# Optimization experiments

Measured on AMD Instinct MI355X. Metric: run time of the kernel, lower is better.

## Reference

```python
import jax, jax.numpy as jnp
import numpy as np

B, S, D, N, H = 2, 1024, 1024, 16, 64
R = 2 * S          # max relative length
EPS = 1e-9
INF = 1000000.0
SHIFT = 1          # q_len == context_len branch


def _forward(query, key, value, r, cls_mask, Wq, Wk, bk, Wv, bv, Wo, bo,
             r_w_bias, r_r_bias, r_kernel, r_s_bias, seg_embed, ln_gamma, ln_beta,
             token_type_mat, attention_mask):
    scale = 1.0 / np.sqrt(H).astype(np.float32)
    q = (query @ Wq).reshape(B, S, N, H) * scale          # [b,s,n,h]
    k = (key @ Wk + bk).reshape(B, S, N, H)
    v = (value @ Wv + bv).reshape(B, S, N, H)

    # content score
    content = jnp.einsum('binh,bjnh->bnij', q + r_w_bias * scale, k)

    # relative positional score with shift-gather trick
    r_head = jnp.einsum('td,dnh->tnh', r, r_kernel)        # [2S,n,h]
    pos = jnp.einsum('binh,tnh->bnit', q + r_r_bias * scale, r_head)  # [b,n,s,2S]
    pos = pos.reshape(B, N, R, S)[:, :, SHIFT:, :].reshape(B, N, S, R - SHIFT)[..., :S]
    pos = pos * cls_mask

    # token-type (segment) score: seg_embed[0]=diff, seg_embed[1]=same
    tt_bias = jnp.einsum('binh,snh->bnis', q + r_s_bias * scale, seg_embed)  # [b,n,s,2]
    diff, same = tt_bias[..., :1], tt_bias[..., 1:]
    tt = jnp.where(token_type_mat[:, None], same, diff) * cls_mask           # [b,n,s,s]

    mask = attention_mask.astype(jnp.float32)[:, None, None]                 # [b,1,1,s]
    attn_score = content + pos + tt - INF * (1.0 - mask)
    attn_prob = jax.nn.softmax(attn_score, axis=-1)

    attn_vec = jnp.einsum('bnij,bjnh->binh', attn_prob, v).reshape(B, S, N * H)
    attn_out = attn_vec @ Wo + bo

    x = query + attn_out
    mu = jnp.mean(x, axis=-1, keepdims=True)
    var = jnp.mean(jnp.square(x - mu), axis=-1, keepdims=True)
    return (x - mu) * jax.lax.rsqrt(var + EPS) * ln_gamma + ln_beta


def setup_inputs() -> dict:
    rng = jax.random.key(0)
    ks = jax.random.split(rng, 16)
    init = 0.02
    inp = {
        'query': jax.random.normal(ks[0], (B, S, D), jnp.float32),
        'key':   jax.random.normal(ks[1], (B, S, D), jnp.float32),
        'value': jax.random.normal(ks[2], (B, S, D), jnp.float32),
        'r':     jax.random.normal(ks[3], (R, D), jnp.float32),
        'cls_mask': jnp.ones((S, S), jnp.float32),
        'Wq': jax.random.normal(ks[4], (D, N * H), jnp.float32) * init,
        'Wk': jax.random.normal(ks[5], (D, N * H), jnp.float32) * init,
        'bk': jnp.zeros((N * H,), jnp.float32),
        'Wv': jax.random.normal(ks[6], (D, N * H), jnp.float32) * init,
        'bv': jnp.zeros((N * H,), jnp.float32),
        'Wo': jax.random.normal(ks[7], (N * H, D), jnp.float32) * init,
        'bo': jnp.zeros((D,), jnp.float32),
        'r_w_bias': jax.random.normal(ks[8], (N, H), jnp.float32) * init,
        'r_r_bias': jax.random.normal(ks[9], (N, H), jnp.float32) * init,
        'r_kernel': jax.random.normal(ks[10], (D, N, H), jnp.float32) * init,
        'r_s_bias': jax.random.normal(ks[11], (N, H), jnp.float32) * init,
        'seg_embed': jax.random.normal(ks[12], (2, N, H), jnp.float32) * init,
        'ln_gamma': jnp.ones((D,), jnp.float32),
        'ln_beta': jnp.zeros((D,), jnp.float32),
        'token_type_mat': jax.random.randint(ks[13], (B, S, S), 0, 2).astype(bool),
        'attention_mask': jax.random.randint(ks[14], (B, S), 0, 2).astype(jnp.int32),
    }
    return inp


def reference(query, key, value, r, cls_mask, Wq, Wk, bk, Wv, bv, Wo, bo,
              r_w_bias, r_r_bias, r_kernel, r_s_bias, seg_embed, ln_gamma, ln_beta,
              token_type_mat, attention_mask):
    return _forward(query, key, value, r, cls_mask, Wq, Wk, bk, Wv, bv, Wo, bo,
                    r_w_bias, r_r_bias, r_kernel, r_s_bias, seg_embed, ln_gamma, ln_beta,
                    token_type_mat, attention_mask)
```

## Files before the change

### kernel.cpp

```cpp
#include <hip/hip_runtime.h>

#define S_ 1024

typedef short short8 __attribute__((ext_vector_type(8)));
typedef float floatx4 __attribute__((ext_vector_type(4)));

static __device__ __forceinline__ float b2f(ushort u) {
    union { float f; unsigned int i; } x; x.i = ((unsigned int)u) << 16; return x.f;
}
static __device__ __forceinline__ ushort f2b(float f) {
    union { float f; unsigned int i; } x; x.f = f;
    unsigned int r = (x.i + 0x7fffu + ((x.i >> 16) & 1u)) >> 16;
    return (ushort)r;
}
static __device__ __forceinline__ void async_copy16(ushort* lds, const ushort* g) {
    __builtin_amdgcn_global_load_lds((const __attribute__((address_space(1))) void*)g,
                                     (__attribute__((address_space(3))) void*)lds, 16, 0, 0);
}
template <int CTRL>
static __device__ __forceinline__ float dpp_radd(float x) {
    union { float f; int i; } a, b;
    a.f = x;
    b.i = __builtin_amdgcn_mov_dpp(a.i, CTRL, 0xf, 0xf, true);
    return x + b.f;
}

struct PreArgs {
    const float* csrc[4]; ushort* cdst[4];
    const float* tsrc[5]; ushort* tdst[5];
    const int* ttm; unsigned long long* ttb;
    const int* am;  unsigned long long* amb;
};
__global__ __launch_bounds__(256) void pre_kernel(PreArgs a) {
    int z = blockIdx.z, tid = threadIdx.x;
    if (z < 4) {
        const float* s = a.csrc[z];
        ushort* d = a.cdst[z];
        size_t idx = ((size_t)blockIdx.x * 256 + tid) * 8;
        float4 f0 = *(const float4*)&s[idx];
        float4 f1 = *(const float4*)&s[idx + 4];
        alignas(16) ushort u[8] = {f2b(f0.x), f2b(f0.y), f2b(f0.z), f2b(f0.w),
                                   f2b(f1.x), f2b(f1.y), f2b(f1.z), f2b(f1.w)};
        *(uint4*)&d[idx] = *(uint4*)u;
    } else if (z < 9) {
        const float* src = a.tsrc[z - 4];
        ushort* dst = a.tdst[z - 4];
        __shared__ float tile[32][33];
        int bx = (blockIdx.x & 31) * 32, by = (blockIdx.x >> 5) * 32;
        int tx = tid & 31, ty = tid >> 5;
#pragma unroll
        for (int i = 0; i < 32; i += 8)
            tile[ty + i][tx] = src[(size_t)(by + ty + i) * 1024 + bx + tx];
        __syncthreads();
#pragma unroll
        for (int i = 0; i < 32; i += 8)
            dst[(size_t)(bx + ty + i) * 1024 + by + tx] = f2b(tile[tx][ty + i]);
    } else {
        int w = tid >> 6, lane = tid & 63;
        int waveid = blockIdx.x * 4 + w;
#pragma unroll
        for (int t = 0; t < 8; t++) {
            int word = waveid * 8 + t;
            unsigned long long m = __ballot(a.ttm[(size_t)word * 64 + lane] != 0);
            if (lane == 0) a.ttb[word] = m;
        }
        if (blockIdx.x == 0 && w == 0) {
            for (int t = 0; t < 32; t++) {
                unsigned long long m = __ballot(a.am[(size_t)t * 64 + lane] != 0);
                if (lane == 0) a.amb[t] = m;
            }
        }
    }
}

struct ProjArgs {
    const ushort* A[4];
    const ushort* BT[4];
    const float* bias[4];
    ushort* C[4];
    float scale[4];
};
__global__ __launch_bounds__(256, 2) void gemm_proj(ProjArgs args) {
    int z = blockIdx.z;
    const ushort* A = args.A[z];
    const ushort* BT = args.BT[z];
    const float* bias = args.bias[z];
    ushort* C = args.C[z];
    float scale = args.scale[z];

    __shared__ alignas(16) ushort As[128 * 64];
    __shared__ alignas(16) ushort Bs[128 * 64];
    int n0 = blockIdx.x * 128, m0 = blockIdx.y * 128;
    int tid = threadIdx.x, lane = tid & 63, w = tid >> 6;
    int wm = (w >> 1) * 64, wn = (w & 1) * 64;
    int li = lane & 15, q4 = lane >> 4;
    int lrow = lane >> 3, lu = (lane & 7) ^ lrow;
    floatx4 acc[4][4] = {};
    for (int k0 = 0; k0 < 1024; k0 += 64) {
        __syncthreads();
#pragma unroll
        for (int t = 0; t < 4; t++) {
            int c = 4 * w + t;
            const ushort* ga = &A[(size_t)(m0 + 8 * c + lrow) * 1024 + k0 + 8 * lu];
            async_copy16(&As[c * 512 + lane * 8], ga);
            const ushort* gb = &BT[(size_t)(n0 + 8 * c + lrow) * 1024 + k0 + 8 * lu];
            async_copy16(&Bs[c * 512 + lane * 8], gb);
        }
        __syncthreads();
        short8 af[2][4], bf[2][4];
#pragma unroll
        for (int kk = 0; kk < 2; kk++) {
#pragma unroll
            for (int ms = 0; ms < 4; ms++)
                af[kk][ms] = *(const short8*)&As[(wm + 16 * ms + li) * 64 +
                                                (((4 * kk + q4) ^ (li & 7)) * 8)];
#pragma unroll
            for (int ns = 0; ns < 4; ns++)
                bf[kk][ns] = *(const short8*)&Bs[(wn + 16 * ns + li) * 64 +
                                                (((4 * kk + q4) ^ (li & 7)) * 8)];
        }
#pragma unroll
        for (int kk = 0; kk < 2; kk++)
#pragma unroll
            for (int ms = 0; ms < 4; ms++)
#pragma unroll
                for (int ns = 0; ns < 4; ns++)
                    acc[ms][ns] = __builtin_amdgcn_mfma_f32_16x16x32_bf16(af[kk][ms], bf[kk][ns],
                                                                          acc[ms][ns], 0, 0, 0);
    }
#pragma unroll
    for (int ns = 0; ns < 4; ns++) {
        int col = n0 + wn + 16 * ns + li;
        float bv = bias ? bias[col] : 0.f;
#pragma unroll
        for (int ms = 0; ms < 4; ms++)
#pragma unroll
            for (int rg = 0; rg < 4; rg++) {
                int row = m0 + wm + 16 * ms + 4 * q4 + rg;
                C[(size_t)row * 1024 + col] = f2b(acc[ms][ns][rg] * scale + bv);
            }
    }
}

__global__ __launch_bounds__(256, 2) void gemm_out(const ushort* __restrict__ A,
                                                   const ushort* __restrict__ BT,
                                                   const float* __restrict__ bias,
                                                   const float* __restrict__ resid,
                                                   float* __restrict__ X) {
    __shared__ alignas(16) ushort As[64 * 64];
    __shared__ alignas(16) ushort Bs[64 * 64];
    int n0 = blockIdx.x * 64, m0 = blockIdx.y * 64;
    int tid = threadIdx.x, lane = tid & 63, w = tid >> 6;
    int wm = (w >> 1) * 32, wn = (w & 1) * 32;
    int li = lane & 15, q4 = lane >> 4;
    int lrow = lane >> 3, lu = (lane & 7) ^ lrow;
    floatx4 acc[2][2] = {};
    for (int k0 = 0; k0 < 1024; k0 += 64) {
        __syncthreads();
#pragma unroll
        for (int t = 0; t < 2; t++) {
            int c = 2 * w + t;
            const ushort* ga = &A[(size_t)(m0 + 8 * c + lrow) * 1024 + k0 + 8 * lu];
            async_copy16(&As[c * 512 + lane * 8], ga);
            const ushort* gb = &BT[(size_t)(n0 + 8 * c + lrow) * 1024 + k0 + 8 * lu];
            async_copy16(&Bs[c * 512 + lane * 8], gb);
        }
        __syncthreads();
        short8 af[2][2], bf[2][2];
#pragma unroll
        for (int kk = 0; kk < 2; kk++) {
#pragma unroll
            for (int ms = 0; ms < 2; ms++)
                af[kk][ms] = *(const short8*)&As[(wm + 16 * ms + li) * 64 +
                                                (((4 * kk + q4) ^ (li & 7)) * 8)];
#pragma unroll
            for (int ns = 0; ns < 2; ns++)
                bf[kk][ns] = *(const short8*)&Bs[(wn + 16 * ns + li) * 64 +
                                                (((4 * kk + q4) ^ (li & 7)) * 8)];
        }
#pragma unroll
        for (int kk = 0; kk < 2; kk++)
#pragma unroll
            for (int ms = 0; ms < 2; ms++)
#pragma unroll
                for (int ns = 0; ns < 2; ns++)
                    acc[ms][ns] = __builtin_amdgcn_mfma_f32_16x16x32_bf16(af[kk][ms], bf[kk][ns],
                                                                          acc[ms][ns], 0, 0, 0);
    }
#pragma unroll
    for (int ns = 0; ns < 2; ns++) {
        int col = n0 + wn + 16 * ns + li;
        float bv = bias[col];
#pragma unroll
        for (int ms = 0; ms < 2; ms++)
#pragma unroll
            for (int rg = 0; rg < 4; rg++) {
                int row = m0 + wm + 16 * ms + 4 * q4 + rg;
                X[(size_t)row * 1024 + col] = acc[ms][ns][rg] + bv + resid[(size_t)row * 1024 + col];
            }
    }
}

__global__ __launch_bounds__(256, 2) void attn_kernel(
    const ushort* __restrict__ qg, const ushort* __restrict__ kg,
    const ushort* __restrict__ vg, const ushort* __restrict__ rh,
    const float* __restrict__ rwb, const float* __restrict__ rrb,
    const float* __restrict__ rsb, const float* __restrict__ seg,
    const unsigned long long* __restrict__ ttb, const unsigned long long* __restrict__ amb,
    ushort* __restrict__ av) {
    __shared__ alignas(16) ushort vt[64][72];
    __shared__ alignas(16) ushort pb[4][16][72];

    int lid = blockIdx.x + 16 * blockIdx.y + 256 * blockIdx.z;
    int g = lid & 7, tt_ = lid >> 3;
    int i0 = (tt_ & 15) * 64;
    int slice = 4 * g + (tt_ >> 4);
    int n = slice & 15, b = slice >> 4;

    int tid = threadIdx.x, lane = tid & 63, w = tid >> 6;
    int li = lane & 15, q4 = lane >> 4;
    const float SC = 0.125f;
    const int kRow = b * S_;

    short8 aw0, aw1, ar0, ar1;
    float ttd_l[4], tts_l[4];
    {
        int qrow = kRow + i0 + 16 * w + li;
        int h0 = n * 64 + 8 * q4;
        const ushort* qp = &qg[(size_t)qrow * 1024 + h0];
        alignas(16) ushort t0[8], t1[8];
        *(uint4*)t0 = *(const uint4*)qp;
        *(uint4*)t1 = *(const uint4*)(qp + 32);
        alignas(16) ushort w0[8], w1[8], r0[8], r1[8];
        float d = 0.f, s = 0.f;
#pragma unroll
        for (int e = 0; e < 8; e++) {
            float qv0 = b2f(t0[e]), qv1 = b2f(t1[e]);
            int ha = h0 + e, hb = h0 + 32 + e;
            w0[e] = f2b(qv0 + rwb[ha] * SC);
            w1[e] = f2b(qv1 + rwb[hb] * SC);
            r0[e] = f2b(qv0 + rrb[ha] * SC);
            r1[e] = f2b(qv1 + rrb[hb] * SC);
            float s0 = qv0 + rsb[ha] * SC, s1 = qv1 + rsb[hb] * SC;
            d += s0 * seg[ha] + s1 * seg[hb];
            s += s0 * seg[1024 + ha] + s1 * seg[1024 + hb];
        }
        aw0 = *(short8*)w0; aw1 = *(short8*)w1;
        ar0 = *(short8*)r0; ar1 = *(short8*)r1;
        d += __shfl_xor(d, 16, 64); d += __shfl_xor(d, 32, 64);
        s += __shfl_xor(s, 16, 64); s += __shfl_xor(s, 32, 64);
#pragma unroll
        for (int r = 0; r < 4; r++) {
            int srcl = (lane & 48) | (4 * q4 + r);
            ttd_l[r] = __shfl(d, srcl, 64);
            tts_l[r] = __shfl(s, srcl, 64);
        }
    }

    floatx4 o[4] = {};
    float l_i[4] = {0.f, 0.f, 0.f, 0.f};

    int g8 = tid >> 5, jp = tid & 31;

    short8 kf0[4], kf1[4], rf0[5], rf1[5];
    uint4 pv0, pv1;
    unsigned long long ptb[4], pamb;

#define LOAD_K(J0)                                                                     \
    {                                                                                  \
        _Pragma("unroll") for (int s_ = 0; s_ < 4; s_++) {                             \
            const ushort* kp =                                                         \
                &kg[(size_t)(kRow + (J0) + 16 * s_ + li) * 1024 + n * 64 + 8 * q4];    \
            kf0[s_] = *(const short8*)kp;                                              \
            kf1[s_] = *(const short8*)(kp + 32);                                       \
        }                                                                              \
    }
#define LOAD_R(J0)                                                                     \
    {                                                                                  \
        _Pragma("unroll") for (int s_ = 0; s_ < 5; s_++) {                             \
            int t_ = 1024 + (J0) - i0 - 15 - 16 * w + 16 * s_ + li;                    \
            if (t_ > 2047) t_ = 2047;                                                  \
            const ushort* rp = &rh[(size_t)t_ * 1024 + n * 64 + 8 * q4];               \
            rf0[s_] = *(const short8*)rp;                                              \
            rf1[s_] = *(const short8*)(rp + 32);                                       \
        }                                                                              \
    }
#define LOAD_VTB(J0)                                                                   \
    {                                                                                  \
        const ushort* vp = &vg[(size_t)(kRow + (J0) + 2 * jp) * 1024 + n * 64 + 8 * g8]; \
        pv0 = *(const uint4*)vp;                                                       \
        pv1 = *(const uint4*)(vp + 1024);                                              \
        int wj_ = (J0) >> 6;                                                           \
        pamb = amb[b * 16 + wj_];                                                      \
        _Pragma("unroll") for (int r_ = 0; r_ < 4; r_++)                               \
            ptb[r_] = ttb[((size_t)kRow + i0 + 16 * w + 4 * q4 + r_) * 16 + wj_];      \
    }
    LOAD_K(0);
    LOAD_R(0);
    LOAD_VTB(0);

    for (int j0 = 0; j0 < 1024; j0 += 64) {
        __syncthreads();
        {
            alignas(16) ushort au[8], bu[8];
            *(uint4*)au = pv0; *(uint4*)bu = pv1;
#pragma unroll
            for (int e = 0; e < 8; e++) {
                unsigned int val = (unsigned int)au[e] | ((unsigned int)bu[e] << 16);
                *(unsigned int*)&vt[8 * g8 + e][2 * jp] = val;
            }
        }
        unsigned long long ambw = pamb;
        unsigned long long tb[4] = {ptb[0], ptb[1], ptb[2], ptb[3]};
        __syncthreads();
        bool more = (j0 + 64 < 1024);
        if (more) LOAD_VTB(j0 + 64);

        floatx4 cs[4] = {};
#pragma unroll
        for (int s = 0; s < 4; s++) {
            cs[s] = __builtin_amdgcn_mfma_f32_16x16x32_bf16(aw0, kf0[s], cs[s], 0, 0, 0);
            cs[s] = __builtin_amdgcn_mfma_f32_16x16x32_bf16(aw1, kf1[s], cs[s], 0, 0, 0);
        }
        if (more) LOAD_K(j0 + 64);

        floatx4 pz[5] = {};
#pragma unroll
        for (int s5 = 0; s5 < 5; s5++) {
            pz[s5] = __builtin_amdgcn_mfma_f32_16x16x32_bf16(ar0, rf0[s5], pz[s5], 0, 0, 0);
            pz[s5] = __builtin_amdgcn_mfma_f32_16x16x32_bf16(ar1, rf1[s5], pz[s5], 0, 0, 0);
        }
        if (more) LOAD_R(j0 + 64);

        float p[4][4];
#pragma unroll
        for (int r = 0; r < 4; r++) {
            int delta = 15 - 4 * q4 - r;
            int srcl = (lane & 48) | ((li + delta) & 15);
            float psum = 0.f;
#pragma unroll
            for (int s = 0; s < 4; s++) {
                float sel = (li < delta) ? pz[s + 1][r] : pz[s][r];
                float posv = __shfl(sel, srcl, 64);
                float ttv = ((tb[r] >> (16 * s + li)) & 1) ? tts_l[r] : ttd_l[r];
                float mbv = ((ambw >> (16 * s + li)) & 1) ? 0.f : -1e6f;
                float sc = cs[s][r] + posv + ttv + mbv;
                p[r][s] = __expf(sc);
                psum += p[r][s];
            }
            psum = dpp_radd<0xB1>(psum);
            psum = dpp_radd<0x4E>(psum);
            psum = dpp_radd<0x124>(psum);
            psum = dpp_radd<0x128>(psum);
            l_i[r] += psum;
        }
#pragma unroll
        for (int r = 0; r < 4; r++)
#pragma unroll
            for (int s = 0; s < 4; s++) pb[w][4 * q4 + r][16 * s + li] = f2b(p[r][s]);
#pragma unroll
        for (int ka = 0; ka < 2; ka++) {
            short8 ap = *(const short8*)&pb[w][li][32 * ka + 8 * q4];
#pragma unroll
            for (int hsub = 0; hsub < 4; hsub++) {
                short8 bv = *(const short8*)&vt[16 * hsub + li][32 * ka + 8 * q4];
                o[hsub] = __builtin_amdgcn_mfma_f32_16x16x32_bf16(ap, bv, o[hsub], 0, 0, 0);
            }
        }
    }
#pragma unroll
    for (int hsub = 0; hsub < 4; hsub++)
#pragma unroll
        for (int r = 0; r < 4; r++) {
            int i = i0 + 16 * w + 4 * q4 + r;
            int h = 16 * hsub + li;
            av[(size_t)(kRow + i) * 1024 + n * 64 + h] = f2b(o[hsub][r] / l_i[r]);
        }
#undef LOAD_K
#undef LOAD_R
#undef LOAD_VTB
}

__global__ __launch_bounds__(256) void ln_kernel(const float* __restrict__ X,
                                                 const float* __restrict__ gamma,
                                                 const float* __restrict__ beta,
                                                 float* __restrict__ out) {
    int row = blockIdx.x, tid = threadIdx.x;
    float4 v = *(const float4*)&X[(size_t)row * 1024 + tid * 4];
    float sum = v.x + v.y + v.z + v.w;
    float sq = v.x * v.x + v.y * v.y + v.z * v.z + v.w * v.w;
#pragma unroll
    for (int off = 32; off >= 1; off >>= 1) {
        sum += __shfl_xor(sum, off, 64);
        sq += __shfl_xor(sq, off, 64);
    }
    __shared__ float rs[4], rq[4];
    int w = tid >> 6;
    if ((tid & 63) == 0) { rs[w] = sum; rq[w] = sq; }
    __syncthreads();
    sum = rs[0] + rs[1] + rs[2] + rs[3];
    sq = rq[0] + rq[1] + rq[2] + rq[3];
    float mu = sum * (1.f / 1024.f);
    float var = sq * (1.f / 1024.f) - mu * mu;
    float rstd = rsqrtf(fmaxf(var, 0.f) + 1e-9f);
    float4 g = *(const float4*)&gamma[tid * 4];
    float4 be = *(const float4*)&beta[tid * 4];
    float4 o;
    o.x = (v.x - mu) * rstd * g.x + be.x;
    o.y = (v.y - mu) * rstd * g.y + be.y;
    o.z = (v.z - mu) * rstd * g.z + be.z;
    o.w = (v.w - mu) * rstd * g.w + be.w;
    *(float4*)&out[(size_t)row * 1024 + tid * 4] = o;
}

extern "C" void kernel_launch(void* const* d_in, const int* in_sizes, int n_in,
                              void* d_out, int out_size, void* d_ws, size_t ws_size,
                              hipStream_t stream) {
    const float* query = (const float*)d_in[0];
    const float* key   = (const float*)d_in[1];
    const float* value = (const float*)d_in[2];
    const float* r     = (const float*)d_in[3];
    const float* Wq  = (const float*)d_in[5];
    const float* Wk  = (const float*)d_in[6];
    const float* bk  = (const float*)d_in[7];
    const float* Wv  = (const float*)d_in[8];
    const float* bv  = (const float*)d_in[9];
    const float* Wo  = (const float*)d_in[10];
    const float* bo  = (const float*)d_in[11];
    const float* rwb = (const float*)d_in[12];
    const float* rrb = (const float*)d_in[13];
    const float* rk  = (const float*)d_in[14];
    const float* rsb = (const float*)d_in[15];
    const float* seg = (const float*)d_in[16];
    const float* gamma = (const float*)d_in[17];
    const float* beta  = (const float*)d_in[18];
    const int* ttm = (const int*)d_in[19];
    const int* am  = (const int*)d_in[20];
    float* out = (float*)d_out;

    char* ws = (char*)d_ws;
    const size_t MB = (size_t)1 << 20;
    ushort* WqT = (ushort*)(ws + 0 * MB);
    ushort* WkT = (ushort*)(ws + 2 * MB);
    ushort* WvT = (ushort*)(ws + 4 * MB);
    ushort* rkT = (ushort*)(ws + 6 * MB);
    ushort* WoT = (ushort*)(ws + 8 * MB);
    ushort* qf  = (ushort*)(ws + 10 * MB);
    ushort* kf  = (ushort*)(ws + 14 * MB);
    ushort* vf  = (ushort*)(ws + 18 * MB);
    ushort* qb  = (ushort*)(ws + 22 * MB);
    ushort* kb  = (ushort*)(ws + 26 * MB);
    ushort* vb  = (ushort*)(ws + 30 * MB);
    unsigned long long* ttb = (unsigned long long*)(ws + 34 * MB);
    unsigned long long* amb = (unsigned long long*)(ws + 34 * MB + 512 * 1024);
    float*  X   = (float*)(ws + 10 * MB);
    ushort* rf  = (ushort*)d_out;
    ushort* avb = (ushort*)d_out;
    ushort* rhb = (ushort*)((char*)d_out + 4 * MB);

    PreArgs pr;
    pr.csrc[0] = query; pr.csrc[1] = key; pr.csrc[2] = value; pr.csrc[3] = r;
    pr.cdst[0] = qf; pr.cdst[1] = kf; pr.cdst[2] = vf; pr.cdst[3] = rf;
    pr.tsrc[0] = Wq; pr.tsrc[1] = Wk; pr.tsrc[2] = Wv; pr.tsrc[3] = rk; pr.tsrc[4] = Wo;
    pr.tdst[0] = WqT; pr.tdst[1] = WkT; pr.tdst[2] = WvT; pr.tdst[3] = rkT; pr.tdst[4] = WoT;
    pr.ttm = ttm; pr.ttb = ttb; pr.am = am; pr.amb = amb;
    pre_kernel<<<dim3(1024, 1, 10), 256, 0, stream>>>(pr);

    ProjArgs pa;
    pa.A[0] = qf; pa.BT[0] = WqT; pa.bias[0] = nullptr; pa.C[0] = qb;  pa.scale[0] = 0.125f;
    pa.A[1] = kf; pa.BT[1] = WkT; pa.bias[1] = bk;      pa.C[1] = kb;  pa.scale[1] = 1.0f;
    pa.A[2] = vf; pa.BT[2] = WvT; pa.bias[2] = bv;      pa.C[2] = vb;  pa.scale[2] = 1.0f;
    pa.A[3] = rf; pa.BT[3] = rkT; pa.bias[3] = nullptr; pa.C[3] = rhb; pa.scale[3] = 1.0f;
    gemm_proj<<<dim3(8, 16, 4), 256, 0, stream>>>(pa);

    attn_kernel<<<dim3(16, 16, 2), 256, 0, stream>>>(qb, kb, vb, rhb, rwb, rrb, rsb, seg,
                                                     ttb, amb, avb);

    gemm_out<<<dim3(16, 32), 256, 0, stream>>>(avb, WoT, bo, query, X);
    ln_kernel<<<2048, 256, 0, stream>>>(X, gamma, beta, out);
}
```

Measured before the change: 280.5 us.

## Stage K and relative-position tiles in swizzled LDS shared across waves

```diff
diff --git a/kernel.cpp b/kernel.cpp
--- a/kernel.cpp
+++ b/kernel.cpp
@@ -208,6 +208,8 @@
     const float* __restrict__ rsb, const float* __restrict__ seg,
     const unsigned long long* __restrict__ ttb, const unsigned long long* __restrict__ amb,
     ushort* __restrict__ av) {
+    __shared__ alignas(16) ushort kt[64][64];
+    __shared__ alignas(16) ushort rwin[128][64];
     __shared__ alignas(16) ushort vt[64][72];
     __shared__ alignas(16) ushort pb[4][16][72];
 
@@ -221,6 +223,7 @@
     int li = lane & 15, q4 = lane >> 4;
     const float SC = 0.125f;
     const int kRow = b * S_;
+    const int x7 = li & 7;
 
     short8 aw0, aw1, ar0, ar1;
     float ttd_l[4], tts_l[4];
@@ -259,48 +262,39 @@
 
     floatx4 o[4] = {};
     float l_i[4] = {0.f, 0.f, 0.f, 0.f};
-
+    const int woff = 48 - 16 * w;
+
+    int kr = tid >> 2;
+    int ku0 = (2 * (tid & 3)) ^ (kr & 7), ku1 = (2 * (tid & 3) + 1) ^ (kr & 7);
     int g8 = tid >> 5, jp = tid & 31;
-
-    short8 kf0[4], kf1[4], rf0[5], rf1[5];
-    uint4 pv0, pv1;
+    int rr = tid >> 1, rb4 = 4 * (tid & 1);
+    int ru0 = (rb4 + 0) ^ (rr & 7), ru1 = (rb4 + 1) ^ (rr & 7);
+    int ru2 = (rb4 + 2) ^ (rr & 7), ru3 = (rb4 + 3) ^ (rr & 7);
+
+    uint4 pk0, pk1, pv0, pv1, pr0, pr1, pr2, pr3;
     unsigned long long ptb[4], pamb;
-
-#define LOAD_K(J0)                                                                     \
-    {                                                                                  \
-        _Pragma("unroll") for (int s_ = 0; s_ < 4; s_++) {                             \
-            const ushort* kp =                                                         \
-                &kg[(size_t)(kRow + (J0) + 16 * s_ + li) * 1024 + n * 64 + 8 * q4];    \
-            kf0[s_] = *(const short8*)kp;                                              \
-            kf1[s_] = *(const short8*)(kp + 32);                                       \
-        }                                                                              \
-    }
-#define LOAD_R(J0)                                                                     \
-    {                                                                                  \
-        _Pragma("unroll") for (int s_ = 0; s_ < 5; s_++) {                             \
-            int t_ = 1024 + (J0) - i0 - 15 - 16 * w + 16 * s_ + li;                    \
-            if (t_ > 2047) t_ = 2047;                                                  \
-            const ushort* rp = &rh[(size_t)t_ * 1024 + n * 64 + 8 * q4];               \
-            rf0[s_] = *(const short8*)rp;                                              \
-            rf1[s_] = *(const short8*)(rp + 32);                                       \
-        }                                                                              \
-    }
-#define LOAD_VTB(J0)                                                                   \
-    {                                                                                  \
-        const ushort* vp = &vg[(size_t)(kRow + (J0) + 2 * jp) * 1024 + n * 64 + 8 * g8]; \
-        pv0 = *(const uint4*)vp;                                                       \
-        pv1 = *(const uint4*)(vp + 1024);                                              \
-        int wj_ = (J0) >> 6;                                                           \
-        pamb = amb[b * 16 + wj_];                                                      \
-        _Pragma("unroll") for (int r_ = 0; r_ < 4; r_++)                               \
-            ptb[r_] = ttb[((size_t)kRow + i0 + 16 * w + 4 * q4 + r_) * 16 + wj_];      \
-    }
-    LOAD_K(0);
-    LOAD_R(0);
-    LOAD_VTB(0);
+#define PREFETCH(J0)                                                                       \
+    {                                                                                      \
+        const ushort* kp = &kg[(size_t)(kRow + (J0) + kr) * 1024 + n * 64 + (tid & 3) * 16]; \
+        pk0 = *(const uint4*)kp; pk1 = *(const uint4*)(kp + 8);                            \
+        const ushort* vp = &vg[(size_t)(kRow + (J0) + 2 * jp) * 1024 + n * 64 + 8 * g8];   \
+        pv0 = *(const uint4*)vp; pv1 = *(const uint4*)(vp + 1024);                         \
+        int t_ = 1024 + (J0) - i0 - 63 + rr;                                               \
+        if (t_ > 2047) t_ = 2047;                                                          \
+        const ushort* rp = &rh[(size_t)t_ * 1024 + n * 64 + 32 * (tid & 1)];               \
+        pr0 = *(const uint4*)&rp[0];  pr1 = *(const uint4*)&rp[8];                         \
+        pr2 = *(const uint4*)&rp[16]; pr3 = *(const uint4*)&rp[24];                        \
+        int wj_ = (J0) >> 6;                                                               \
+        pamb = amb[b * 16 + wj_];                                                          \
+        _Pragma("unroll") for (int r_ = 0; r_ < 4; r_++)                                   \
+            ptb[r_] = ttb[((size_t)kRow + i0 + 16 * w + 4 * q4 + r_) * 16 + wj_];          \
+    }
+    PREFETCH(0);
 
     for (int j0 = 0; j0 < 1024; j0 += 64) {
         __syncthreads();
+        *(uint4*)&kt[kr][8 * ku0] = pk0;
+        *(uint4*)&kt[kr][8 * ku1] = pk1;
         {
             alignas(16) ushort au[8], bu[8];
             *(uint4*)au = pv0; *(uint4*)bu = pv1;
@@ -310,27 +304,32 @@
                 *(unsigned int*)&vt[8 * g8 + e][2 * jp] = val;
             }
         }
+        *(uint4*)&rwin[rr][8 * ru0] = pr0;
+        *(uint4*)&rwin[rr][8 * ru1] = pr1;
+        *(uint4*)&rwin[rr][8 * ru2] = pr2;
+        *(uint4*)&rwin[rr][8 * ru3] = pr3;
         unsigned long long ambw = pamb;
         unsigned long long tb[4] = {ptb[0], ptb[1], ptb[2], ptb[3]};
         __syncthreads();
-        bool more = (j0 + 64 < 1024);
-        if (more) LOAD_VTB(j0 + 64);
+        if (j0 + 64 < 1024) PREFETCH(j0 + 64);
 
         floatx4 cs[4] = {};
 #pragma unroll
         for (int s = 0; s < 4; s++) {
-            cs[s] = __builtin_amdgcn_mfma_f32_16x16x32_bf16(aw0, kf0[s], cs[s], 0, 0, 0);
-            cs[s] = __builtin_amdgcn_mfma_f32_16x16x32_bf16(aw1, kf1[s], cs[s], 0, 0, 0);
-        }
-        if (more) LOAD_K(j0 + 64);
-
+            short8 b0 = *(const short8*)&kt[16 * s + li][8 * (q4 ^ x7)];
+            short8 b1 = *(const short8*)&kt[16 * s + li][8 * ((q4 + 4) ^ x7)];
+            cs[s] = __builtin_amdgcn_mfma_f32_16x16x32_bf16(aw0, b0, cs[s], 0, 0, 0);
+            cs[s] = __builtin_amdgcn_mfma_f32_16x16x32_bf16(aw1, b1, cs[s], 0, 0, 0);
+        }
         floatx4 pz[5] = {};
 #pragma unroll
         for (int s5 = 0; s5 < 5; s5++) {
-            pz[s5] = __builtin_amdgcn_mfma_f32_16x16x32_bf16(ar0, rf0[s5], pz[s5], 0, 0, 0);
-            pz[s5] = __builtin_amdgcn_mfma_f32_16x16x32_bf16(ar1, rf1[s5], pz[s5], 0, 0, 0);
-        }
-        if (more) LOAD_R(j0 + 64);
+            const ushort* rw = &rwin[woff + 16 * s5 + li][0];
+            short8 b0 = *(const short8*)&rw[8 * (q4 ^ x7)];
+            short8 b1 = *(const short8*)&rw[8 * ((q4 + 4) ^ x7)];
+            pz[s5] = __builtin_amdgcn_mfma_f32_16x16x32_bf16(ar0, b0, pz[s5], 0, 0, 0);
+            pz[s5] = __builtin_amdgcn_mfma_f32_16x16x32_bf16(ar1, b1, pz[s5], 0, 0, 0);
+        }
 
         float p[4][4];
 #pragma unroll
@@ -376,9 +375,7 @@
             int h = 16 * hsub + li;
             av[(size_t)(kRow + i) * 1024 + n * 64 + h] = f2b(o[hsub][r] / l_i[r]);
         }
-#undef LOAD_K
-#undef LOAD_R
-#undef LOAD_VTB
+#undef PREFETCH
 }
 
 __global__ __launch_bounds__(256) void ln_kernel(const float* __restrict__ X,
```

Result: faster. 233.5 us (-16.8%).
